# Kernel tuning notes

Hardware: AMD Instinct MI355X
Metric: run time of the kernel (lower is better)

## Reference

```python
import jax, jax.numpy as jnp
import numpy as np

B, C, N = 2, 256, 8192
H = W = 64
C4 = C // 4
EPS = 1e-5


def bn(x, gamma, beta, mean, var):
    # eval-mode batchnorm over channel axis 1
    shape = (1, -1) + (1,) * (x.ndim - 2)
    inv = gamma * jax.lax.rsqrt(var + EPS)
    return x * inv.reshape(shape) + (beta - mean * inv).reshape(shape)


def conv1x1(x, w, b):
    # w: (Cout, Cin)
    return jnp.einsum('bchw,oc->bohw', x, w) + b.reshape(1, -1, 1, 1)


def conv2d(x, w, b=None, padding='VALID', groups=1, lhs_dilation=None):
    y = jax.lax.conv_general_dilated(
        x, w, window_strides=(1, 1), padding=padding,
        lhs_dilation=lhs_dilation, feature_group_count=groups,
        dimension_numbers=('NCHW', 'OIHW', 'NCHW'))
    return y if b is None else y + b.reshape(1, -1, 1, 1)


def lift_net(x, w1, b1, w2, b2, axis):
    # DAWN predictor/updater: ReflectionPad(2,1) -> conv k=4 along axis (C4->2C4)
    # -> ReLU -> 1x1 conv (2C4->C4) -> Tanh
    pad = [(0, 0)] * 4
    pad[axis] = (2, 1)
    xp = jnp.pad(x, pad, mode='reflect')
    k = w1[:, :, None, :] if axis == 3 else w1[:, :, :, None]
    h = jax.nn.relu(conv2d(xp, k, b1))
    return jnp.tanh(conv1x1(h, w2, b2))


def lifting(x, pw, axis):
    # pw = (w1, b1, w2, b2), each with leading net axis [P, U]
    w1, b1, w2, b2 = pw
    sl_e = [slice(None)] * 4; sl_e[axis] = slice(0, None, 2)
    sl_o = [slice(None)] * 4; sl_o[axis] = slice(1, None, 2)
    x_even, x_odd = x[tuple(sl_e)], x[tuple(sl_o)]
    d = x_odd - lift_net(x_even, w1[0], b1[0], w2[0], b2[0], axis)
    c = x_even + lift_net(d, w1[1], b1[1], w2[1], b2[1], axis)
    return c, d


def wavelet2d(x, w1, b1, w2, b2):
    # leading axes of weights: (scheme[horizontal, vertical], net[P, U])
    c, d = lifting(x, (w1[0], b1[0], w2[0], b2[0]), axis=3)  # split along W
    v = (w1[1], b1[1], w2[1], b2[1])                          # shared vertical weights
    LL, LH = lifting(c, v, axis=2)
    HL, HH = lifting(d, v, axis=2)
    return LL, LH, HL, HH


def convT(x, w, b):
    # torch ConvTranspose2d(k=4, stride=2, pad=1); w: (Cin, Cout, 4, 4)
    wc = jnp.flip(w, (2, 3)).transpose(1, 0, 2, 3)  # (Cout, Cin, 4, 4)
    return conv2d(x, wc, b, padding=[(2, 2), (2, 2)], lhs_dilation=(2, 2))


def _forward(tokens, flatten_mat, bn_gamma, bn_beta, bn_mean, bn_var, red_w, red_b,
             lift_w1, lift_b1, lift_w2, lift_b2,
             ff2_w1, ff2_b1, ff2_w2, ff2_b2, ct2_w, ct2_b,
             bn2_gamma, bn2_beta, bn2_mean, bn2_var,
             ff1_w1, ff1_b1, ff1_w2, ff1_b2, ct1_w, ct1_b,
             bn1_gamma, bn1_beta, bn1_mean, bn1_var,
             dw1_w, dw1_b, dw2_w, dw2_b, scale_w, inflate_idx):
    r = bn(tokens, bn_gamma, bn_beta, bn_mean, bn_var)                       # (B,C,N)
    r = jnp.einsum('bmn,bcn->bcm', flatten_mat, r).reshape(B, C, H, W)       # flatten to grid
    rr = conv1x1(r, red_w, red_b)                                            # (B,C/4,H,W)
    LL1, LH1, HL1, HH1 = wavelet2d(rr, lift_w1[0], lift_b1[0], lift_w2[0], lift_b2[0])
    LL2, LH2, HL2, HH2 = wavelet2d(LL1, lift_w1[1], lift_b1[1], lift_w2[1], lift_b2[1])
    x2 = jnp.concatenate([LL2, LH2, HL2, HH2], 1)                            # (B,C,H/4,W/4)
    y2 = conv1x1(jax.nn.gelu(conv1x1(x2, ff2_w1, ff2_b1), approximate=False), ff2_w2, ff2_b2)
    y2 = bn(convT(y2, ct2_w, ct2_b), bn2_gamma, bn2_beta, bn2_mean, bn2_var) # (B,C/2,H/2,W/2)
    x1 = jnp.concatenate([LL1, LH1, HL1, HH1, y2], 1)                        # (B,1.5C,H/2,W/2)
    y1 = conv1x1(jax.nn.gelu(conv1x1(x1, ff1_w1, ff1_b1), approximate=False), ff1_w2, ff1_b2)
    y1 = bn(convT(y1, ct1_w, ct1_b), bn1_gamma, bn1_beta, bn1_mean, bn1_var) # (B,C,H,W)
    r = r + y1
    r = conv2d(r, dw1_w, dw1_b, padding=[(1, 1), (1, 1)], groups=C)          # depthwise 3x3
    r = conv2d(jax.nn.relu(r), dw2_w, dw2_b, padding=[(1, 1), (1, 1)], groups=C)
    r = r.reshape(B, C, H * W) * scale_w.reshape(1, C, 1)                    # grouped 1x1 conv1d
    r = jnp.take_along_axis(r, inflate_idx, axis=2)                          # inflate gather
    return tokens + r


def setup_inputs() -> dict:
    key = jax.random.key(0)
    ks = iter(jax.random.split(key, 64))
    nrm = lambda shape, s=0.05: jax.random.normal(next(ks), shape, jnp.float32) * s
    uni = lambda shape: jax.random.uniform(next(ks), shape, jnp.float32, 0.5, 1.5)
    return dict(
        tokens=jax.random.normal(next(ks), (B, C, N), jnp.float32),
        flatten_mat=nrm((B, H * W, N), 0.02),
        inflate_idx=jax.random.randint(next(ks), (B, C, N), 0, H * W),
        bn_gamma=jnp.ones((C,), jnp.float32), bn_beta=jnp.zeros((C,), jnp.float32),
        bn_mean=nrm((C,), 0.1), bn_var=uni((C,)),
        red_w=nrm((C4, C)), red_b=nrm((C4,)),
        lift_w1=nrm((2, 2, 2, 2 * C4, C4, 4)), lift_b1=nrm((2, 2, 2, 2 * C4)),
        lift_w2=nrm((2, 2, 2, C4, 2 * C4)), lift_b2=nrm((2, 2, 2, C4)),
        ff2_w1=nrm((C, C)), ff2_b1=nrm((C,)), ff2_w2=nrm((C, C)), ff2_b2=nrm((C,)),
        ct2_w=nrm((C, C // 2, 4, 4)), ct2_b=nrm((C // 2,)),
        bn2_gamma=jnp.ones((C // 2,), jnp.float32), bn2_beta=jnp.zeros((C // 2,), jnp.float32),
        bn2_mean=nrm((C // 2,), 0.1), bn2_var=uni((C // 2,)),
        ff1_w1=nrm((C, C + C // 2)), ff1_b1=nrm((C,)), ff1_w2=nrm((C, C)), ff1_b2=nrm((C,)),
        ct1_w=nrm((C, C, 4, 4)), ct1_b=nrm((C,)),
        bn1_gamma=jnp.ones((C,), jnp.float32), bn1_beta=jnp.zeros((C,), jnp.float32),
        bn1_mean=nrm((C,), 0.1), bn1_var=uni((C,)),
        dw1_w=nrm((C, 1, 3, 3)), dw1_b=nrm((C,)),
        dw2_w=nrm((C, 1, 3, 3)), dw2_b=nrm((C,)),
        scale_w=nrm((C,), 0.2),
    )


def reference(tokens, flatten_mat, inflate_idx, bn_gamma, bn_beta, bn_mean, bn_var,
              red_w, red_b, lift_w1, lift_b1, lift_w2, lift_b2,
              ff2_w1, ff2_b1, ff2_w2, ff2_b2, ct2_w, ct2_b,
              bn2_gamma, bn2_beta, bn2_mean, bn2_var,
              ff1_w1, ff1_b1, ff1_w2, ff1_b2, ct1_w, ct1_b,
              bn1_gamma, bn1_beta, bn1_mean, bn1_var,
              dw1_w, dw1_b, dw2_w, dw2_b, scale_w):
    return _forward(tokens, flatten_mat, bn_gamma, bn_beta, bn_mean, bn_var, red_w, red_b,
                    lift_w1, lift_b1, lift_w2, lift_b2,
                    ff2_w1, ff2_b1, ff2_w2, ff2_b2, ct2_w, ct2_b,
                    bn2_gamma, bn2_beta, bn2_mean, bn2_var,
                    ff1_w1, ff1_b1, ff1_w2, ff1_b2, ct1_w, ct1_b,
                    bn1_gamma, bn1_beta, bn1_mean, bn1_var,
                    dw1_w, dw1_b, dw2_w, dw2_b, scale_w, inflate_idx)
```

## Files before the change

kernel.cpp:

```cpp
#include <hip/hip_runtime.h>
#include <math.h>

#define EPSV 1e-5f

typedef __attribute__((ext_vector_type(8))) short bf16x8;
typedef __attribute__((ext_vector_type(4))) float f32x4;
typedef __attribute__((ext_vector_type(8))) unsigned short u16x8;

__device__ inline unsigned short f2bf(float f) {
    unsigned u = __float_as_uint(f);
    unsigned r = (u + 0x7fffu + ((u >> 16) & 1u)) >> 16;
    return (unsigned short)r;
}

__device__ inline float bf2f(unsigned short h) {
    return __uint_as_float(((unsigned)h) << 16);
}

__device__ inline void gload_lds16(const void* g, void* l) {
    __builtin_amdgcn_global_load_lds(
        (const __attribute__((address_space(1))) void*)g,
        (__attribute__((address_space(3))) void*)l, 16, 0, 0);
}

__device__ void wpack_item(const float* __restrict__ w, unsigned short* __restrict__ wp,
                           int Cout, int Cin, int id)
{
    int nc8 = Cin >> 3;
    int cch = id % nc8;
    int rest = id / nc8;
    int o = rest % Cout;
    int pt = rest / Cout;
    if (pt >= 16) return;
    int par = pt >> 2, tap = pt & 3;
    int py = par >> 1, px = par & 1, u = tap >> 1, v = tap & 1;
    int tf = (3 - py - 2 * u) * 4 + (3 - px - 2 * v);
    u16x8 h;
    #pragma unroll
    for (int e = 0; e < 8; ++e)
        h[e] = f2bf(w[((cch * 8 + e) * Cout + o) * 16 + tf]);
    *reinterpret_cast<u16x8*>(&wp[((pt * Cout + o) * Cin) + cch * 8]) = h;
}

__global__ __launch_bounds__(256) void prep_kernel(
    const float4* __restrict__ x, ushort4* __restrict__ y,
    const float* __restrict__ g, const float* __restrict__ be,
    const float* __restrict__ mu, const float* __restrict__ va,
    const float* __restrict__ ct1w, unsigned short* __restrict__ wp1,
    const float* __restrict__ ct2w, unsigned short* __restrict__ wp2)
{
    int vb = blockIdx.x, t = threadIdx.x;
    if (vb < 4096) {
        int i = vb * 256 + t;
        int c = (i >> 11) & 255;
        float s = g[c] * rsqrtf(va[c] + EPSV);
        float tt = be[c] - mu[c] * s;
        float4 v = x[i];
        ushort4 h;
        h.x = f2bf(v.x * s + tt); h.y = f2bf(v.y * s + tt);
        h.z = f2bf(v.z * s + tt); h.w = f2bf(v.w * s + tt);
        y[i] = h;
    } else if (vb < 4608) {
        wpack_item(ct1w, wp1, 256, 256, (vb - 4096) * 256 + t);
    } else {
        wpack_item(ct2w, wp2, 128, 256, (vb - 4608) * 256 + t);
    }
}

__global__ __launch_bounds__(256) void flatten_gemm_mfma(
    const unsigned short* __restrict__ A, const float* __restrict__ Bm,
    float* __restrict__ Pbase)
{
    __shared__ __align__(16) unsigned short AS[4][256 * 32];
    __shared__ __align__(16) unsigned short BS[4][64 * 32];
    const int NTT = 64;
    int t = threadIdx.x;
    int wid = t >> 6, lane = t & 63;
    int fid = blockIdx.z * 64 + blockIdx.x;
    int nid = (fid & 7) * 64 + (fid >> 3);
    int n0 = (nid & 63) * 64;
    int zz = nid >> 6;
    int ks = zz & 3, b = zz >> 2;
    const unsigned short* Ab = A + b * (256 * 8192);
    const float* Bb = Bm + (long)b * (4096 * 8192) + (long)n0 * 8192;
    int k0 = ks * 2048;
    int brow = t >> 3, bc8 = t & 7;
    int l15 = lane & 15, kc = lane >> 4;

    f32x4 acc[4][4] = {};

    auto issueA = [&](int tile) {
        int buf = tile & 3;
        int kb = k0 + tile * 32;
        #pragma unroll
        for (int j = 0; j < 4; ++j) {
            int d16 = (wid * 4 + j) * 64 + lane;
            int row = d16 >> 2;
            int ch = (d16 & 3) ^ ((row >> 1) & 3);
            gload_lds16(Ab + row * 8192 + kb + ch * 8, &AS[buf][(wid * 4 + j) * 512]);
        }
    };
    auto loadB = [&](int tile, float4& f0, float4& f1) {
        int kb = k0 + tile * 32;
        f0 = *(const float4*)(Bb + brow * 8192 + kb + bc8 * 4);
        f1 = *(const float4*)(Bb + (brow + 32) * 8192 + kb + bc8 * 4);
    };
    auto writeB = [&](int tile, const float4& f0, const float4& f1) {
        int buf = tile & 3;
        int ch16 = (bc8 >> 1) ^ ((brow >> 1) & 3);
        ushort4 h;
        h.x = f2bf(f0.x); h.y = f2bf(f0.y); h.z = f2bf(f0.z); h.w = f2bf(f0.w);
        *reinterpret_cast<ushort4*>(&BS[buf][brow * 32 + ch16 * 8 + (bc8 & 1) * 4]) = h;
        int rr2 = brow + 32;
        int ch16b = (bc8 >> 1) ^ ((rr2 >> 1) & 3);
        ushort4 h2;
        h2.x = f2bf(f1.x); h2.y = f2bf(f1.y); h2.z = f2bf(f1.z); h2.w = f2bf(f1.w);
        *reinterpret_cast<ushort4*>(&BS[buf][rr2 * 32 + ch16b * 8 + (bc8 & 1) * 4]) = h2;
    };
    auto mmac = [&](int tile) {
        int buf = tile & 3;
        bf16x8 af[4], bfr[4];
        #pragma unroll
        for (int mf = 0; mf < 4; ++mf) {
            int row = wid * 64 + mf * 16 + l15;
            int ch = kc ^ ((row >> 1) & 3);
            af[mf] = *reinterpret_cast<const bf16x8*>(&AS[buf][row * 32 + ch * 8]);
        }
        #pragma unroll
        for (int nf = 0; nf < 4; ++nf) {
            int row = nf * 16 + l15;
            int ch = kc ^ ((row >> 1) & 3);
            bfr[nf] = *reinterpret_cast<const bf16x8*>(&BS[buf][row * 32 + ch * 8]);
        }
        #pragma unroll
        for (int mf = 0; mf < 4; ++mf)
            #pragma unroll
            for (int nf = 0; nf < 4; ++nf)
                acc[mf][nf] = __builtin_amdgcn_mfma_f32_16x16x32_bf16(
                    af[mf], bfr[nf], acc[mf][nf], 0, 0, 0);
    };

    float4 q00, q01, q10, q11, r0, r1;
    loadB(0, q00, q01);
    loadB(1, q10, q11);
    issueA(0);
    issueA(1);

    for (int tau = 0; tau < NTT; ++tau) {
        writeB(tau, q00, q01);
        if (tau == 0)
            asm volatile("s_waitcnt vmcnt(4) lgkmcnt(0)" ::: "memory");
        else if (tau < NTT - 1)
            asm volatile("s_waitcnt vmcnt(6) lgkmcnt(0)" ::: "memory");
        else
            asm volatile("s_waitcnt vmcnt(0) lgkmcnt(0)" ::: "memory");
        __builtin_amdgcn_s_barrier();
        if (tau + 2 < NTT) {
            loadB(tau + 2, r0, r1);
            issueA(tau + 2);
        }
        mmac(tau);
        q00 = q10; q01 = q11; q10 = r0; q11 = r1;
    }

    float* P = Pbase + (long)ks * 2097152;
    float* Cb = P + (b * 256) * 4096 + n0;
    #pragma unroll
    for (int mf = 0; mf < 4; ++mf) {
        int rbase = wid * 64 + mf * 16 + (lane >> 4) * 4;
        #pragma unroll
        for (int nf = 0; nf < 4; ++nf) {
            int col = nf * 16 + (lane & 15);
            #pragma unroll
            for (int r = 0; r < 4; ++r)
                Cb[(rbase + r) * 4096 + col] = acc[mf][nf][r];
        }
    }
}

__global__ __launch_bounds__(256) void add4_t_kernel(
    const float* __restrict__ p, unsigned short* __restrict__ obf)
{
    __shared__ float tl[64][65];
    int t = threadIdx.x;
    int b = blockIdx.z;
    int c0 = blockIdx.y * 64, p0 = blockIdx.x * 64;
    #pragma unroll
    for (int u = 0; u < 16; ++u) {
        int idx = u * 256 + t;
        int cl = idx >> 6, pl = idx & 63;
        long g = (long)(b * 256 + c0 + cl) * 4096 + p0 + pl;
        tl[cl][pl] = p[g] + p[g + 2097152] + p[g + 2 * 2097152] + p[g + 3 * 2097152];
    }
    __syncthreads();
    #pragma unroll
    for (int u = 0; u < 16; ++u) {
        int idx = u * 256 + t;
        int pl = idx >> 6, cl = idx & 63;
        obf[(long)(b * 4096 + p0 + pl) * 256 + c0 + cl] = f2bf(tl[cl][pl]);
    }
}

template<int NF>
__global__ __launch_bounds__(256) void conv1x1_mfma(
    const unsigned short* __restrict__ xbf, const float* __restrict__ w,
    const float* __restrict__ bias, float* __restrict__ of32,
    unsigned short* __restrict__ obf, int Cin, int Cout, int P, int act)
{
    constexpr int BP = NF * 64;
    __shared__ __align__(16) unsigned short XS[2][BP * 32];
    __shared__ __align__(16) unsigned short WS[2][64 * 32];
    int t = threadIdx.x;
    int wid = t >> 6, lane = t & 63;
    int b = blockIdx.z;
    int p0 = blockIdx.x * BP, o0 = blockIdx.y * 64;
    const unsigned short* xb = xbf + (long)b * P * Cin;
    int wm = t >> 2, wq = t & 3;
    int chunks = Cin >> 5;

    f32x4 acc[4][NF] = {};

    #pragma unroll
    for (int j = 0; j < NF; ++j) {
        int d16 = (wid * NF + j) * 64 + lane;
        int p = d16 >> 2;
        int ch = (d16 & 3) ^ ((p >> 1) & 3);
        gload_lds16(xb + (long)(p0 + p) * Cin + ch * 8, &XS[0][(wid * NF + j) * 512]);
    }
    float4 wr0 = *(const float4*)(w + (o0 + wm) * Cin + wq * 8);
    float4 wr1 = *(const float4*)(w + (o0 + wm) * Cin + wq * 8 + 4);
    __syncthreads();

    for (int cc = 0; cc < chunks; ++cc) {
        int cur = cc & 1;
        {
            int chq = wq ^ ((wm >> 1) & 3);
            u16x8 h;
            h[0] = f2bf(wr0.x); h[1] = f2bf(wr0.y); h[2] = f2bf(wr0.z); h[3] = f2bf(wr0.w);
            h[4] = f2bf(wr1.x); h[5] = f2bf(wr1.y); h[6] = f2bf(wr1.z); h[7] = f2bf(wr1.w);
            *reinterpret_cast<u16x8*>(&WS[cur][wm * 32 + chq * 8]) = h;
        }
        __syncthreads();

        if (cc < chunks - 1) {
            int kn = (cc + 1) * 32;
            #pragma unroll
            for (int j = 0; j < NF; ++j) {
                int d16 = (wid * NF + j) * 64 + lane;
                int p = d16 >> 2;
                int ch = (d16 & 3) ^ ((p >> 1) & 3);
                gload_lds16(xb + (long)(p0 + p) * Cin + kn + ch * 8,
                            &XS[cur ^ 1][(wid * NF + j) * 512]);
            }
            wr0 = *(const float4*)(w + (o0 + wm) * Cin + kn + wq * 8);
            wr1 = *(const float4*)(w + (o0 + wm) * Cin + kn + wq * 8 + 4);
        }

        int l15 = lane & 15, kc = lane >> 4;
        bf16x8 af[4], bfr[NF];
        #pragma unroll
        for (int mf = 0; mf < 4; ++mf) {
            int row = mf * 16 + l15;
            int ch = kc ^ ((row >> 1) & 3);
            af[mf] = *reinterpret_cast<const bf16x8*>(&WS[cur][row * 32 + ch * 8]);
        }
        #pragma unroll
        for (int nf = 0; nf < NF; ++nf) {
            int row = wid * (NF * 16) + nf * 16 + l15;
            int ch = kc ^ ((row >> 1) & 3);
            bfr[nf] = *reinterpret_cast<const bf16x8*>(&XS[cur][row * 32 + ch * 8]);
        }
        #pragma unroll
        for (int mf = 0; mf < 4; ++mf)
            #pragma unroll
            for (int nf = 0; nf < NF; ++nf)
                acc[mf][nf] = __builtin_amdgcn_mfma_f32_16x16x32_bf16(
                    af[mf], bfr[nf], acc[mf][nf], 0, 0, 0);
        __syncthreads();
    }

    int l15 = lane & 15, kc4 = lane >> 4;
    #pragma unroll
    for (int mf = 0; mf < 4; ++mf) {
        #pragma unroll
        for (int nf = 0; nf < NF; ++nf) {
            int p = wid * (NF * 16) + nf * 16 + l15;
            ushort4 hb;
            #pragma unroll
            for (int r = 0; r < 4; ++r) {
                int m = mf * 16 + kc4 * 4 + r;
                float v = acc[mf][nf][r] + bias[o0 + m];
                if (act == 1) v = fmaxf(v, 0.f);
                else if (act == 2) v = 0.5f * v * (1.f + erff(v * 0.70710678118f));
                if (of32) of32[((long)(b * Cout) + o0 + m) * P + p0 + p] = v;
                ((unsigned short*)&hb)[r] = f2bf(v);
            }
            if (obf)
                *reinterpret_cast<ushort4*>(
                    &obf[(long)(b * P + p0 + p) * Cout + o0 + mf * 16 + kc4 * 4]) = hb;
        }
    }
}

__global__ __launch_bounds__(256) void convt_mfma(
    const unsigned short* __restrict__ xbf, const unsigned short* __restrict__ wp,
    const float* __restrict__ bias, const float* __restrict__ g,
    const float* __restrict__ be, const float* __restrict__ mu,
    const float* __restrict__ va, const unsigned short* __restrict__ resbf,
    float* __restrict__ of32, unsigned short* __restrict__ obf,
    int Cin, int Cout, int Hin, int Win, int TR, int cshift, int OCtot, int cof)
{
    __shared__ __align__(16) unsigned short XS[165 * 32];
    __shared__ __align__(16) unsigned short WS[4 * 64 * 32];
    int t = threadIdx.x;
    int wid = t >> 6, lane = t & 63;
    int z = blockIdx.z;
    int b = z >> 2, par = z & 3;
    int py = par >> 1, px = par & 1;
    int o0 = blockIdx.y * 64;
    int i0 = blockIdx.x * TR;
    int CW = Win, CW1 = CW + 1;
    int npatch = (TR + 1) * CW1;
    int Pin = Hin * Win, Pout = 4 * Hin * Win;
    const unsigned short* xb = xbf + (long)b * Pin * Cin;
    int chunks = Cin >> 5;
    int l15 = lane & 15, kc = lane >> 4;

    f32x4 acc[4][2] = {};

    for (int cc = 0; cc < chunks; ++cc) {
        __syncthreads();
        for (int idx = t; idx < npatch * 4; idx += 256) {
            int pp = idx >> 2, ql = idx & 3;
            int qs = ql ^ ((pp >> 1) & 3);
            int a = pp / CW1, bcol = pp - a * CW1;
            int iy = i0 - (1 - py) + a;
            int ix = bcol - (1 - px);
            u16x8 v = {};
            if (iy >= 0 && iy < Hin && ix >= 0 && ix < Win)
                v = *reinterpret_cast<const u16x8*>(
                    &xb[(long)(iy * Win + ix) * Cin + cc * 32 + qs * 8]);
            *reinterpret_cast<u16x8*>(&XS[pp * 32 + ql * 8]) = v;
        }
        {
            int m = t >> 2, q = t & 3;
            int chq = q ^ ((m >> 1) & 3);
            #pragma unroll
            for (int tap = 0; tap < 4; ++tap) {
                u16x8 v = *reinterpret_cast<const u16x8*>(
                    &wp[((long)((par * 4 + tap) * Cout + o0 + m)) * Cin + cc * 32 + q * 8]);
                *reinterpret_cast<u16x8*>(&WS[tap * 2048 + m * 32 + chq * 8]) = v;
            }
        }
        __syncthreads();

        #pragma unroll
        for (int tap = 0; tap < 4; ++tap) {
            int u = tap >> 1, v = tap & 1;
            bf16x8 af[4], bfr[2];
            #pragma unroll
            for (int mf = 0; mf < 4; ++mf) {
                int row = mf * 16 + l15;
                int ch = kc ^ ((row >> 1) & 3);
                af[mf] = *reinterpret_cast<const bf16x8*>(&WS[tap * 2048 + row * 32 + ch * 8]);
            }
            #pragma unroll
            for (int nf = 0; nf < 2; ++nf) {
                int n = wid * 32 + nf * 16 + l15;
                int rn = n >> cshift, cn = n & (CW - 1);
                int pp = (rn + u) * CW1 + cn + v;
                int ch = kc ^ ((pp >> 1) & 3);
                bfr[nf] = *reinterpret_cast<const bf16x8*>(&XS[pp * 32 + ch * 8]);
            }
            #pragma unroll
            for (int mf = 0; mf < 4; ++mf)
                #pragma unroll
                for (int nf = 0; nf < 2; ++nf)
                    acc[mf][nf] = __builtin_amdgcn_mfma_f32_16x16x32_bf16(
                        af[mf], bfr[nf], acc[mf][nf], 0, 0, 0);
        }
    }

    int kc4 = lane >> 4;
    #pragma unroll
    for (int nf = 0; nf < 2; ++nf) {
        int n = wid * 32 + nf * 16 + l15;
        int rn = n >> cshift, cn = n & (CW - 1);
        int y = 2 * (i0 + rn) + py;
        int xx = 2 * cn + px;
        int pout = y * 2 * Win + xx;
        #pragma unroll
        for (int mf = 0; mf < 4; ++mf) {
            ushort4 hb;
            #pragma unroll
            for (int r = 0; r < 4; ++r) {
                int m = mf * 16 + kc4 * 4 + r;
                int o = o0 + m;
                float s = g[o] * rsqrtf(va[o] + EPSV);
                float v = (acc[mf][nf][r] + bias[o]) * s + (be[o] - mu[o] * s);
                if (resbf) v += bf2f(resbf[(long)(b * Pout + pout) * 256 + o]);
                if (of32) of32[((long)(b * Cout) + o) * Pout + pout] = v;
                ((unsigned short*)&hb)[r] = f2bf(v);
            }
            if (obf)
                *reinterpret_cast<ushort4*>(
                    &obf[(long)(b * Pout + pout) * OCtot + cof + o0 + mf * 16 + kc4 * 4]) = hb;
        }
    }
}

__global__ __launch_bounds__(1024) void lift_net_kernel(
    const float* __restrict__ xA, const float* __restrict__ xB,
    const float* __restrict__ oA, const float* __restrict__ oB,
    float* __restrict__ uA, float* __restrict__ uB,
    int x_sB, int x_sC, int x_sR, int x_sA,
    int o_sB, int o_sC, int o_sR, int o_sA,
    int u_sB, int u_sC, int u_sR, int u_sA,
    const float* __restrict__ w1, const float* __restrict__ b1,
    const float* __restrict__ w2, const float* __restrict__ b2,
    int R, int L, int lsh, float sign,
    unsigned short* __restrict__ obf, int Pb, int OCb, int cofA, int cofB)
{
    __shared__ float xsm[4864];
    __shared__ float hsm[8192];
    int t = threadIdx.x;
    int g = t & 63, ocg = t >> 6;
    int b = blockIdx.z;
    int sel = blockIdx.y;
    const float* xin = sel ? xB : xA;
    const float* oth = sel ? oB : oA;
    float* outp = sel ? uB : uA;
    int cofb = sel ? cofB : cofA;
    int rpb = 64 >> lsh;
    int row0 = blockIdx.x * rpb;
    int Lp = L + 3;
    int total = 64 * rpb * Lp;
    for (int idx = t; idx < total; idx += 1024) {
        int c = idx / (rpb * Lp);
        int rem = idx - c * rpb * Lp;
        int rr_l = rem / Lp;
        int q = rem - rr_l * Lp;
        int s = q - 2;
        s = (s < 0) ? -s : s;
        if (s >= L) s = 2 * L - 2 - s;
        xsm[idx] = xin[b * x_sB + c * x_sC + (row0 + rr_l) * x_sR + s * x_sA];
    }
    __syncthreads();

    int ocgu = __builtin_amdgcn_readfirstlane(ocg);
    int rl = g >> lsh, jl = g & (L - 1);
    const float* w1u = w1 + ocgu * 8 * 256;
    float acc1[8] = {};
    for (int c = 0; c < 64; ++c) {
        const float* xr = &xsm[(c * rpb + rl) * Lp + jl];
        float x0 = xr[0], x1 = xr[1], x2 = xr[2], x3 = xr[3];
        const float* wc = w1u + c * 4;
        #pragma unroll
        for (int k = 0; k < 8; ++k) {
            const float* wr = wc + k * 256;
            acc1[k] += wr[0] * x0 + wr[1] * x1 + wr[2] * x2 + wr[3] * x3;
        }
    }
    #pragma unroll
    for (int k = 0; k < 8; ++k) {
        int oc = ocgu * 8 + k;
        hsm[oc * 64 + g] = fmaxf(acc1[k] + b1[oc], 0.f);
    }
    __syncthreads();

    const float* w2u = w2 + ocgu * 4 * 128;
    float acc2[4] = {};
    for (int h4 = 0; h4 < 32; ++h4) {
        float hv0 = hsm[(h4 * 4 + 0) * 64 + g];
        float hv1 = hsm[(h4 * 4 + 1) * 64 + g];
        float hv2 = hsm[(h4 * 4 + 2) * 64 + g];
        float hv3 = hsm[(h4 * 4 + 3) * 64 + g];
        #pragma unroll
        for (int kk = 0; kk < 4; ++kk) {
            const float* wr = w2u + kk * 128 + h4 * 4;
            acc2[kk] += wr[0] * hv0 + wr[1] * hv1 + wr[2] * hv2 + wr[3] * hv3;
        }
    }
    int rg = row0 + rl;
    int p = rg * u_sR + jl * u_sA;
    #pragma unroll
    for (int kk = 0; kk < 4; ++kk) {
        int o = ocgu * 4 + kk;
        float v = oth[b * o_sB + o * o_sC + rg * o_sR + jl * o_sA]
                + sign * tanhf(acc2[kk] + b2[o]);
        outp[b * u_sB + o * u_sC + p] = v;
        if (obf) obf[(long)(b * Pb + p) * OCb + cofb + o] = f2bf(v);
    }
}

__global__ __launch_bounds__(256) void dw_fused_kernel(
    const float* __restrict__ r2, const float* __restrict__ w1, const float* __restrict__ b1,
    const float* __restrict__ w2, const float* __restrict__ b2v,
    const float* __restrict__ scw, const float* __restrict__ tok,
    const int* __restrict__ idx, float* __restrict__ out)
{
    __shared__ float s0[64][68];
    __shared__ float s1[64][68];
    __shared__ float s2[4096];
    int bc = blockIdx.x;
    int c = bc & 255;
    int t = threadIdx.x;
    const float* xp = r2 + (long)bc * 4096;
    for (int i = t; i < 4096; i += 256) s0[i >> 6][i & 63] = xp[i];
    float wa[9], wb[9];
    #pragma unroll
    for (int k = 0; k < 9; ++k) { wa[k] = w1[c * 9 + k]; wb[k] = w2[c * 9 + k]; }
    float ba = b1[c], bb = b2v[c], sc = scw[c];
    __syncthreads();
    for (int i = t; i < 4096; i += 256) {
        int y = i >> 6, x = i & 63;
        float a = ba;
        #pragma unroll
        for (int ky = 0; ky < 3; ++ky) {
            int yy = y + ky - 1;
            if (yy < 0 || yy > 63) continue;
            #pragma unroll
            for (int kx = 0; kx < 3; ++kx) {
                int xx = x + kx - 1;
                if (xx < 0 || xx > 63) continue;
                a += wa[ky * 3 + kx] * s0[yy][xx];
            }
        }
        s1[y][x] = fmaxf(a, 0.f);
    }
    __syncthreads();
    for (int i = t; i < 4096; i += 256) {
        int y = i >> 6, x = i & 63;
        float a = bb;
        #pragma unroll
        for (int ky = 0; ky < 3; ++ky) {
            int yy = y + ky - 1;
            if (yy < 0 || yy > 63) continue;
            #pragma unroll
            for (int kx = 0; kx < 3; ++kx) {
                int xx = x + kx - 1;
                if (xx < 0 || xx > 63) continue;
                a += wb[ky * 3 + kx] * s1[yy][xx];
            }
        }
        s2[i] = a * sc;
    }
    __syncthreads();
    long base = (long)bc << 13;
    const int4* ip = (const int4*)(idx + base);
    const float4* tp = (const float4*)(tok + base);
    float4* op = (float4*)(out + base);
    for (int i = t; i < 2048; i += 256) {
        int4 iv = ip[i];
        float4 tv = tp[i];
        float4 o;
        o.x = tv.x + s2[iv.x];
        o.y = tv.y + s2[iv.y];
        o.z = tv.z + s2[iv.z];
        o.w = tv.w + s2[iv.w];
        op[i] = o;
    }
}

extern "C" void kernel_launch(void* const* d_in, const int* in_sizes, int n_in,
                              void* d_out, int out_size, void* d_ws, size_t ws_size,
                              hipStream_t stream)
{
    const float* tokens = (const float*)d_in[0];
    const float* fm     = (const float*)d_in[1];
    const int*   infl   = (const int*)d_in[2];
    const float* bng = (const float*)d_in[3];
    const float* bnb = (const float*)d_in[4];
    const float* bnm = (const float*)d_in[5];
    const float* bnv = (const float*)d_in[6];
    const float* red_w = (const float*)d_in[7];
    const float* red_b = (const float*)d_in[8];
    const float* lw1 = (const float*)d_in[9];
    const float* lb1 = (const float*)d_in[10];
    const float* lw2 = (const float*)d_in[11];
    const float* lb2 = (const float*)d_in[12];
    const float* f2w1 = (const float*)d_in[13];
    const float* f2b1 = (const float*)d_in[14];
    const float* f2w2 = (const float*)d_in[15];
    const float* f2b2 = (const float*)d_in[16];
    const float* ct2w = (const float*)d_in[17];
    const float* ct2b = (const float*)d_in[18];
    const float* bn2g = (const float*)d_in[19];
    const float* bn2b = (const float*)d_in[20];
    const float* bn2m = (const float*)d_in[21];
    const float* bn2v = (const float*)d_in[22];
    const float* f1w1 = (const float*)d_in[23];
    const float* f1b1 = (const float*)d_in[24];
    const float* f1w2 = (const float*)d_in[25];
    const float* f1b2 = (const float*)d_in[26];
    const float* ct1w = (const float*)d_in[27];
    const float* ct1b = (const float*)d_in[28];
    const float* bn1g = (const float*)d_in[29];
    const float* bn1b = (const float*)d_in[30];
    const float* bn1m = (const float*)d_in[31];
    const float* bn1v = (const float*)d_in[32];
    const float* dw1w = (const float*)d_in[33];
    const float* dw1b = (const float*)d_in[34];
    const float* dw2w = (const float*)d_in[35];
    const float* dw2b = (const float*)d_in[36];
    const float* scw  = (const float*)d_in[37];

    float* ws = (float*)d_ws;
    unsigned short* Abf = (unsigned short*)ws;
    float* part  = ws + 2097152;
    unsigned short* rgrid_bf = (unsigned short*)(ws + 10485760);
    float* rr    = ws + 11534336;
    float* c1    = ws + 12058624;
    float* d1    = ws + 12320768;
    float* c2    = ws + 12582912;
    float* d2    = ws + 12648448;
    float* x2    = ws + 12713984;
    unsigned short* x2_bf  = (unsigned short*)(ws + 12845056);
    float* x1    = ws + 12910592;
    unsigned short* x1_bf  = (unsigned short*)(ws + 13697024);
    unsigned short* g2_bf  = (unsigned short*)(ws + 14090240);
    unsigned short* y2p_bf = (unsigned short*)(ws + 14155776);
    unsigned short* g1_bf  = (unsigned short*)(ws + 14221312);
    unsigned short* y1p_bf = (unsigned short*)(ws + 14483456);
    unsigned short* wp2    = (unsigned short*)(ws + 14745600);
    unsigned short* wp1    = (unsigned short*)(ws + 15007744);
    float* r2 = ws + 15532032;

    prep_kernel<<<4864, 256, 0, stream>>>((const float4*)tokens, (ushort4*)Abf,
                                          bng, bnb, bnm, bnv, ct1w, wp1, ct2w, wp2);
    flatten_gemm_mfma<<<dim3(64, 1, 8), 256, 0, stream>>>(Abf, fm, part);
    add4_t_kernel<<<dim3(64, 4, 2), 256, 0, stream>>>(part, rgrid_bf);
    conv1x1_mfma<2><<<dim3(32, 1, 2), 256, 0, stream>>>(rgrid_bf, red_w, red_b,
                                                        rr, (unsigned short*)nullptr,
                                                        256, 64, 4096, 0);

    auto lift2 = [&](const float* xA, const float* xB, const float* oA, const float* oB,
                     float* uA, float* uB,
                     int xsB, int xsC, int xsR, int xsA,
                     int osB, int osC, int osR, int osA,
                     int usB, int usC, int usR, int usA,
                     int lvl, int sch, int net, int R, int L, float sign,
                     unsigned short* obf, int Pb, int OCb, int cofA, int cofB, int nsel) {
        int widx = (lvl * 2 + sch) * 2 + net;
        int lsh = (L == 32) ? 5 : 4;
        lift_net_kernel<<<dim3(R * L / 64, nsel, 2), 1024, 0, stream>>>(
            xA, xB, oA, oB, uA, uB,
            xsB, xsC, xsR, xsA, osB, osC, osR, osA, usB, usC, usR, usA,
            lw1 + widx * 32768, lb1 + widx * 128, lw2 + widx * 8192, lb2 + widx * 64,
            R, L, lsh, sign, obf, Pb, OCb, cofA, cofB);
    };

    lift2(rr, rr, rr + 1, rr + 1, d1, d1,
          262144, 4096, 64, 2,  262144, 4096, 64, 2,  131072, 2048, 32, 1,
          0, 0, 0, 64, 32, -1.f, nullptr, 0, 0, 0, 0, 1);
    lift2(d1, d1, rr, rr, c1, c1,
          131072, 2048, 32, 1,  262144, 4096, 64, 2,  131072, 2048, 32, 1,
          0, 0, 1, 64, 32, +1.f, nullptr, 0, 0, 0, 0, 1);
    lift2(c1, d1, c1 + 32, d1 + 32, x1 + 65536, x1 + 196608,
          131072, 2048, 1, 64,  131072, 2048, 1, 64,  393216, 1024, 1, 32,
          0, 1, 0, 32, 32, -1.f, x1_bf, 1024, 384, 64, 192, 2);
    lift2(x1 + 65536, x1 + 196608, c1, d1, x1, x1 + 131072,
          393216, 1024, 1, 32,  131072, 2048, 1, 64,  393216, 1024, 1, 32,
          0, 1, 1, 32, 32, +1.f, x1_bf, 1024, 384, 0, 128, 2);
    lift2(x1, x1, x1 + 1, x1 + 1, d2, d2,
          393216, 1024, 32, 2,  393216, 1024, 32, 2,  65536, 512, 16, 1,
          1, 0, 0, 32, 16, -1.f, nullptr, 0, 0, 0, 0, 1);
    lift2(d2, d2, x1, x1, c2, c2,
          65536, 512, 16, 1,  393216, 1024, 32, 2,  65536, 512, 16, 1,
          1, 0, 1, 32, 16, +1.f, nullptr, 0, 0, 0, 0, 1);
    lift2(c2, d2, c2 + 16, d2 + 16, x2 + 16384, x2 + 49152,
          65536, 512, 1, 32,  65536, 512, 1, 32,  65536, 256, 1, 16,
          1, 1, 0, 16, 16, -1.f, x2_bf, 256, 256, 64, 192, 2);
    lift2(x2 + 16384, x2 + 49152, c2, d2, x2, x2 + 32768,
          65536, 256, 1, 16,  65536, 512, 1, 32,  65536, 256, 1, 16,
          1, 1, 1, 16, 16, +1.f, x2_bf, 256, 256, 0, 128, 2);

    conv1x1_mfma<1><<<dim3(4, 4, 2), 256, 0, stream>>>(x2_bf, f2w1, f2b1,
        (float*)nullptr, g2_bf, 256, 256, 256, 2);
    conv1x1_mfma<1><<<dim3(4, 4, 2), 256, 0, stream>>>(g2_bf, f2w2, f2b2,
        (float*)nullptr, y2p_bf, 256, 256, 256, 0);
    convt_mfma<<<dim3(2, 2, 8), 256, 0, stream>>>(y2p_bf, wp2, ct2b,
        bn2g, bn2b, bn2m, bn2v, (const unsigned short*)nullptr,
        (float*)nullptr, x1_bf, 256, 128, 16, 16, 8, 4, 384, 256);

    conv1x1_mfma<2><<<dim3(8, 4, 2), 256, 0, stream>>>(x1_bf, f1w1, f1b1,
        (float*)nullptr, g1_bf, 384, 256, 1024, 2);
    conv1x1_mfma<2><<<dim3(8, 4, 2), 256, 0, stream>>>(g1_bf, f1w2, f1b2,
        (float*)nullptr, y1p_bf, 256, 256, 1024, 0);
    convt_mfma<<<dim3(8, 4, 8), 256, 0, stream>>>(y1p_bf, wp1, ct1b,
        bn1g, bn1b, bn1m, bn1v, rgrid_bf,
        r2, (unsigned short*)nullptr, 256, 256, 32, 32, 4, 5, 0, 0);

    dw_fused_kernel<<<512, 256, 0, stream>>>(r2, dw1w, dw1b, dw2w, dw2b, scw,
                                             tokens, infl, (float*)d_out);
}
```

Measured before the change: 658.9 us.

## Fuse mid-pipeline kernels into one persistent kernel with grid barriers

Replaces the sequence of add4, reduction conv, eight lifting passes, feed-forward convs and both transposed convs with a single 64-block persistent kernel that synchronises stages through an atomic grid barrier. It targets the cost of many small kernel launches and their inter-kernel gaps. In exchange, each stage runs on only 64 workgroups, some of them with idle sub-groups, so parallelism drops for the larger stages such as the final transposed conv. Correctness also depends on all 64 blocks being co-resident.

```diff
diff --git a/kernel.cpp b/kernel.cpp
--- a/kernel.cpp
+++ b/kernel.cpp
@@ -21,6 +21,23 @@
     __builtin_amdgcn_global_load_lds(
         (const __attribute__((address_space(1))) void*)g,
         (__attribute__((address_space(3))) void*)l, 16, 0, 0);
+}
+
+__device__ __forceinline__ void gridbar(unsigned* cnt, unsigned* gen, unsigned nblk)
+{
+    __syncthreads();
+    if (threadIdx.x == 0) {
+        unsigned g = __hip_atomic_load(gen, __ATOMIC_RELAXED, __HIP_MEMORY_SCOPE_AGENT);
+        unsigned a = __hip_atomic_fetch_add(cnt, 1u, __ATOMIC_ACQ_REL, __HIP_MEMORY_SCOPE_AGENT);
+        if (a == nblk - 1u) {
+            __hip_atomic_store(cnt, 0u, __ATOMIC_RELAXED, __HIP_MEMORY_SCOPE_AGENT);
+            __hip_atomic_fetch_add(gen, 1u, __ATOMIC_ACQ_REL, __HIP_MEMORY_SCOPE_AGENT);
+        } else {
+            while (__hip_atomic_load(gen, __ATOMIC_ACQUIRE, __HIP_MEMORY_SCOPE_AGENT) == g)
+                __builtin_amdgcn_s_sleep(8);
+        }
+    }
+    __syncthreads();
 }
 
 __device__ void wpack_item(const float* __restrict__ w, unsigned short* __restrict__ wp,
@@ -47,9 +64,12 @@
     const float* __restrict__ g, const float* __restrict__ be,
     const float* __restrict__ mu, const float* __restrict__ va,
     const float* __restrict__ ct1w, unsigned short* __restrict__ wp1,
-    const float* __restrict__ ct2w, unsigned short* __restrict__ wp2)
+    const float* __restrict__ ct2w, unsigned short* __restrict__ wp2,
+    unsigned* __restrict__ cnt)
 {
     int vb = blockIdx.x, t = threadIdx.x;
+    if (vb == 0 && t == 0)
+        __hip_atomic_store(cnt, 0u, __ATOMIC_RELAXED, __HIP_MEMORY_SCOPE_AGENT);
     if (vb < 4096) {
         int i = vb * 256 + t;
         int c = (i >> 11) & 255;
@@ -178,44 +198,21 @@
     }
 }
 
-__global__ __launch_bounds__(256) void add4_t_kernel(
-    const float* __restrict__ p, unsigned short* __restrict__ obf)
-{
-    __shared__ float tl[64][65];
-    int t = threadIdx.x;
-    int b = blockIdx.z;
-    int c0 = blockIdx.y * 64, p0 = blockIdx.x * 64;
-    #pragma unroll
-    for (int u = 0; u < 16; ++u) {
-        int idx = u * 256 + t;
-        int cl = idx >> 6, pl = idx & 63;
-        long g = (long)(b * 256 + c0 + cl) * 4096 + p0 + pl;
-        tl[cl][pl] = p[g] + p[g + 2097152] + p[g + 2 * 2097152] + p[g + 3 * 2097152];
-    }
-    __syncthreads();
-    #pragma unroll
-    for (int u = 0; u < 16; ++u) {
-        int idx = u * 256 + t;
-        int pl = idx >> 6, cl = idx & 63;
-        obf[(long)(b * 4096 + p0 + pl) * 256 + c0 + cl] = f2bf(tl[cl][pl]);
-    }
-}
-
 template<int NF>
-__global__ __launch_bounds__(256) void conv1x1_mfma(
+__device__ void conv1x1_body(char* sm, int tt,
     const unsigned short* __restrict__ xbf, const float* __restrict__ w,
     const float* __restrict__ bias, float* __restrict__ of32,
-    unsigned short* __restrict__ obf, int Cin, int Cout, int P, int act)
+    unsigned short* __restrict__ obf, int Cin, int Cout, int P, int act,
+    int bx, int by, int bz)
 {
     constexpr int BP = NF * 64;
-    __shared__ __align__(16) unsigned short XS[2][BP * 32];
-    __shared__ __align__(16) unsigned short WS[2][64 * 32];
-    int t = threadIdx.x;
-    int wid = t >> 6, lane = t & 63;
-    int b = blockIdx.z;
-    int p0 = blockIdx.x * BP, o0 = blockIdx.y * 64;
+    unsigned short* XS = (unsigned short*)sm;
+    unsigned short* WS = XS + 2 * BP * 32;
+    int wid = tt >> 6, lane = tt & 63;
+    int b = bz;
+    int p0 = bx * BP, o0 = by * 64;
     const unsigned short* xb = xbf + (long)b * P * Cin;
-    int wm = t >> 2, wq = t & 3;
+    int wm = tt >> 2, wq = tt & 3;
     int chunks = Cin >> 5;
 
     f32x4 acc[4][NF] = {};
@@ -225,7 +222,7 @@
         int d16 = (wid * NF + j) * 64 + lane;
         int p = d16 >> 2;
         int ch = (d16 & 3) ^ ((p >> 1) & 3);
-        gload_lds16(xb + (long)(p0 + p) * Cin + ch * 8, &XS[0][(wid * NF + j) * 512]);
+        gload_lds16(xb + (long)(p0 + p) * Cin + ch * 8, &XS[(wid * NF + j) * 512]);
     }
     float4 wr0 = *(const float4*)(w + (o0 + wm) * Cin + wq * 8);
     float4 wr1 = *(const float4*)(w + (o0 + wm) * Cin + wq * 8 + 4);
@@ -238,7 +235,7 @@
             u16x8 h;
             h[0] = f2bf(wr0.x); h[1] = f2bf(wr0.y); h[2] = f2bf(wr0.z); h[3] = f2bf(wr0.w);
             h[4] = f2bf(wr1.x); h[5] = f2bf(wr1.y); h[6] = f2bf(wr1.z); h[7] = f2bf(wr1.w);
-            *reinterpret_cast<u16x8*>(&WS[cur][wm * 32 + chq * 8]) = h;
+            *reinterpret_cast<u16x8*>(&WS[cur * 2048 + wm * 32 + chq * 8]) = h;
         }
         __syncthreads();
 
@@ -250,7 +247,7 @@
                 int p = d16 >> 2;
                 int ch = (d16 & 3) ^ ((p >> 1) & 3);
                 gload_lds16(xb + (long)(p0 + p) * Cin + kn + ch * 8,
-                            &XS[cur ^ 1][(wid * NF + j) * 512]);
+                            &XS[(cur ^ 1) * BP * 32 + (wid * NF + j) * 512]);
             }
             wr0 = *(const float4*)(w + (o0 + wm) * Cin + kn + wq * 8);
             wr1 = *(const float4*)(w + (o0 + wm) * Cin + kn + wq * 8 + 4);
@@ -262,13 +259,13 @@
         for (int mf = 0; mf < 4; ++mf) {
             int row = mf * 16 + l15;
             int ch = kc ^ ((row >> 1) & 3);
-            af[mf] = *reinterpret_cast<const bf16x8*>(&WS[cur][row * 32 + ch * 8]);
+            af[mf] = *reinterpret_cast<const bf16x8*>(&WS[cur * 2048 + row * 32 + ch * 8]);
         }
         #pragma unroll
         for (int nf = 0; nf < NF; ++nf) {
             int row = wid * (NF * 16) + nf * 16 + l15;
             int ch = kc ^ ((row >> 1) & 3);
-            bfr[nf] = *reinterpret_cast<const bf16x8*>(&XS[cur][row * 32 + ch * 8]);
+            bfr[nf] = *reinterpret_cast<const bf16x8*>(&XS[cur * BP * 32 + row * 32 + ch * 8]);
         }
         #pragma unroll
         for (int mf = 0; mf < 4; ++mf)
@@ -302,23 +299,22 @@
     }
 }
 
-__global__ __launch_bounds__(256) void convt_mfma(
+__device__ void convt_body(char* sm, int tt,
     const unsigned short* __restrict__ xbf, const unsigned short* __restrict__ wp,
     const float* __restrict__ bias, const float* __restrict__ g,
     const float* __restrict__ be, const float* __restrict__ mu,
     const float* __restrict__ va, const unsigned short* __restrict__ resbf,
     float* __restrict__ of32, unsigned short* __restrict__ obf,
-    int Cin, int Cout, int Hin, int Win, int TR, int cshift, int OCtot, int cof)
-{
-    __shared__ __align__(16) unsigned short XS[165 * 32];
-    __shared__ __align__(16) unsigned short WS[4 * 64 * 32];
-    int t = threadIdx.x;
-    int wid = t >> 6, lane = t & 63;
-    int z = blockIdx.z;
-    int b = z >> 2, par = z & 3;
+    int Cin, int Cout, int Hin, int Win, int TR, int cshift, int OCtot, int cof,
+    int bx, int by, int bz)
+{
+    unsigned short* XS = (unsigned short*)sm;
+    unsigned short* WS = XS + 5280;
+    int wid = tt >> 6, lane = tt & 63;
+    int b = bz >> 2, par = bz & 3;
     int py = par >> 1, px = par & 1;
-    int o0 = blockIdx.y * 64;
-    int i0 = blockIdx.x * TR;
+    int o0 = by * 64;
+    int i0 = bx * TR;
     int CW = Win, CW1 = CW + 1;
     int npatch = (TR + 1) * CW1;
     int Pin = Hin * Win, Pout = 4 * Hin * Win;
@@ -330,7 +326,7 @@
 
     for (int cc = 0; cc < chunks; ++cc) {
         __syncthreads();
-        for (int idx = t; idx < npatch * 4; idx += 256) {
+        for (int idx = tt; idx < npatch * 4; idx += 256) {
             int pp = idx >> 2, ql = idx & 3;
             int qs = ql ^ ((pp >> 1) & 3);
             int a = pp / CW1, bcol = pp - a * CW1;
@@ -343,7 +339,7 @@
             *reinterpret_cast<u16x8*>(&XS[pp * 32 + ql * 8]) = v;
         }
         {
-            int m = t >> 2, q = t & 3;
+            int m = tt >> 2, q = tt & 3;
             int chq = q ^ ((m >> 1) & 3);
             #pragma unroll
             for (int tap = 0; tap < 4; ++tap) {
@@ -409,7 +405,7 @@
     }
 }
 
-__global__ __launch_bounds__(1024) void lift_net_kernel(
+__device__ void lift_body(char* sm, int t, int bx, int sel, int bz,
     const float* __restrict__ xA, const float* __restrict__ xB,
     const float* __restrict__ oA, const float* __restrict__ oB,
     float* __restrict__ uA, float* __restrict__ uB,
@@ -418,21 +414,19 @@
     int u_sB, int u_sC, int u_sR, int u_sA,
     const float* __restrict__ w1, const float* __restrict__ b1,
     const float* __restrict__ w2, const float* __restrict__ b2,
-    int R, int L, int lsh, float sign,
+    int L, int lsh, float sign,
     unsigned short* __restrict__ obf, int Pb, int OCb, int cofA, int cofB)
 {
-    __shared__ float xsm[4864];
-    __shared__ float hsm[8192];
-    int t = threadIdx.x;
+    float* xsm = (float*)sm;
+    float* hsm = xsm + 4864;
     int g = t & 63, ocg = t >> 6;
-    int b = blockIdx.z;
-    int sel = blockIdx.y;
+    int b = bz;
     const float* xin = sel ? xB : xA;
     const float* oth = sel ? oB : oA;
     float* outp = sel ? uB : uA;
     int cofb = sel ? cofB : cofA;
     int rpb = 64 >> lsh;
-    int row0 = blockIdx.x * rpb;
+    int row0 = bx * rpb;
     int Lp = L + 3;
     int total = 64 * rpb * Lp;
     for (int idx = t; idx < total; idx += 1024) {
@@ -490,6 +484,156 @@
                 + sign * tanhf(acc2[kk] + b2[o]);
         outp[b * u_sB + o * u_sC + p] = v;
         if (obf) obf[(long)(b * Pb + p) * OCb + cofb + o] = f2bf(v);
+    }
+}
+
+struct MegaArgs {
+    const float* part;
+    unsigned short* rgrid_bf;
+    const float *red_w, *red_b;
+    float *rr, *c1, *d1, *c2, *d2, *x1, *x2;
+    unsigned short *x1_bf, *x2_bf;
+    const float *lw1, *lb1, *lw2, *lb2;
+    const float *f2w1, *f2b1, *f2w2, *f2b2;
+    unsigned short *g2_bf, *y2p_bf;
+    const unsigned short* wp2;
+    const float *ct2b, *bn2g, *bn2b, *bn2m, *bn2v;
+    const float *f1w1, *f1b1, *f1w2, *f1b2;
+    unsigned short *g1_bf, *y1p_bf;
+    const unsigned short* wp1;
+    const float *ct1b, *bn1g, *bn1b, *bn1m, *bn1v;
+    float* r2;
+    unsigned *cnt, *gen;
+};
+
+__global__ __launch_bounds__(1024) void mega_kernel(MegaArgs A)
+{
+    __shared__ __align__(16) char pool[98304];
+    int vb = blockIdx.x;
+    int t = threadIdx.x;
+    int st = t >> 8, tt = t & 255;
+
+    {
+        float* tl = (float*)pool;
+        for (int r = 0; r < 2; ++r) {
+            int task = r * 64 + vb;
+            int b = task >> 6, p0 = (task & 63) * 64;
+            for (int idx = t; idx < 16384; idx += 1024) {
+                int c = idx >> 6, pl = idx & 63;
+                long g = (long)(b * 256 + c) * 4096 + p0 + pl;
+                tl[c * 66 + pl] = A.part[g] + A.part[g + 2097152]
+                                + A.part[g + 2 * 2097152] + A.part[g + 3 * 2097152];
+            }
+            __syncthreads();
+            for (int idx = t; idx < 16384; idx += 1024) {
+                int pl = idx >> 8, c = idx & 255;
+                A.rgrid_bf[(long)(b * 4096 + p0 + pl) * 256 + c] = f2bf(tl[c * 66 + pl]);
+            }
+            __syncthreads();
+        }
+    }
+    gridbar(A.cnt, A.gen, 64);
+
+    if (vb < 16) {
+        int task = vb * 4 + st;
+        conv1x1_body<2>(pool + st * 24576, tt, A.rgrid_bf, A.red_w, A.red_b,
+                        A.rr, nullptr, 256, 64, 4096, 0, task & 31, 0, task >> 5);
+    }
+    gridbar(A.cnt, A.gen, 64);
+
+    #define WSEG(i) A.lw1 + (i) * 32768, A.lb1 + (i) * 128, A.lw2 + (i) * 8192, A.lb2 + (i) * 64
+    lift_body(pool, t, vb & 31, 0, vb >> 5, A.rr, A.rr, A.rr + 1, A.rr + 1, A.d1, A.d1,
+              262144, 4096, 64, 2, 262144, 4096, 64, 2, 131072, 2048, 32, 1,
+              WSEG(0), 32, 5, -1.f, nullptr, 0, 0, 0, 0);
+    gridbar(A.cnt, A.gen, 64);
+    lift_body(pool, t, vb & 31, 0, vb >> 5, A.d1, A.d1, A.rr, A.rr, A.c1, A.c1,
+              131072, 2048, 32, 1, 262144, 4096, 64, 2, 131072, 2048, 32, 1,
+              WSEG(1), 32, 5, +1.f, nullptr, 0, 0, 0, 0);
+    gridbar(A.cnt, A.gen, 64);
+    lift_body(pool, t, vb & 15, (vb >> 4) & 1, vb >> 5,
+              A.c1, A.d1, A.c1 + 32, A.d1 + 32, A.x1 + 65536, A.x1 + 196608,
+              131072, 2048, 1, 64, 131072, 2048, 1, 64, 393216, 1024, 1, 32,
+              WSEG(2), 32, 5, -1.f, A.x1_bf, 1024, 384, 64, 192);
+    gridbar(A.cnt, A.gen, 64);
+    lift_body(pool, t, vb & 15, (vb >> 4) & 1, vb >> 5,
+              A.x1 + 65536, A.x1 + 196608, A.c1, A.d1, A.x1, A.x1 + 131072,
+              393216, 1024, 1, 32, 131072, 2048, 1, 64, 393216, 1024, 1, 32,
+              WSEG(3), 32, 5, +1.f, A.x1_bf, 1024, 384, 0, 128);
+    gridbar(A.cnt, A.gen, 64);
+    if (vb < 16)
+        lift_body(pool, t, vb & 7, 0, vb >> 3, A.x1, A.x1, A.x1 + 1, A.x1 + 1, A.d2, A.d2,
+                  393216, 1024, 32, 2, 393216, 1024, 32, 2, 65536, 512, 16, 1,
+                  WSEG(4), 16, 4, -1.f, nullptr, 0, 0, 0, 0);
+    gridbar(A.cnt, A.gen, 64);
+    if (vb < 16)
+        lift_body(pool, t, vb & 7, 0, vb >> 3, A.d2, A.d2, A.x1, A.x1, A.c2, A.c2,
+                  65536, 512, 16, 1, 393216, 1024, 32, 2, 65536, 512, 16, 1,
+                  WSEG(5), 16, 4, +1.f, nullptr, 0, 0, 0, 0);
+    gridbar(A.cnt, A.gen, 64);
+    if (vb < 16)
+        lift_body(pool, t, vb & 3, (vb >> 2) & 1, vb >> 3,
+                  A.c2, A.d2, A.c2 + 16, A.d2 + 16, A.x2 + 16384, A.x2 + 49152,
+                  65536, 512, 1, 32, 65536, 512, 1, 32, 65536, 256, 1, 16,
+                  WSEG(6), 16, 4, -1.f, A.x2_bf, 256, 256, 64, 192);
+    gridbar(A.cnt, A.gen, 64);
+    if (vb < 16)
+        lift_body(pool, t, vb & 3, (vb >> 2) & 1, vb >> 3,
+                  A.x2 + 16384, A.x2 + 49152, A.c2, A.d2, A.x2, A.x2 + 32768,
+                  65536, 256, 1, 16, 65536, 512, 1, 32, 65536, 256, 1, 16,
+                  WSEG(7), 16, 4, +1.f, A.x2_bf, 256, 256, 0, 128);
+    gridbar(A.cnt, A.gen, 64);
+    #undef WSEG
+
+    if (vb < 8) {
+        int task = vb * 4 + st;
+        conv1x1_body<1>(pool + st * 16384, tt, A.x2_bf, A.f2w1, A.f2b1,
+                        nullptr, A.g2_bf, 256, 256, 256, 2,
+                        task & 3, (task >> 2) & 3, task >> 4);
+    }
+    gridbar(A.cnt, A.gen, 64);
+    if (vb < 8) {
+        int task = vb * 4 + st;
+        conv1x1_body<1>(pool + st * 16384, tt, A.g2_bf, A.f2w2, A.f2b2,
+                        nullptr, A.y2p_bf, 256, 256, 256, 0,
+                        task & 3, (task >> 2) & 3, task >> 4);
+    }
+    gridbar(A.cnt, A.gen, 64);
+    if (vb < 16) {
+        if (st < 2) {
+            int task = vb * 2 + st;
+            convt_body(pool + st * 27008, tt, A.y2p_bf, A.wp2, A.ct2b,
+                       A.bn2g, A.bn2b, A.bn2m, A.bn2v, nullptr,
+                       nullptr, A.x1_bf, 256, 128, 16, 16, 8, 4, 384, 256,
+                       task & 1, (task >> 1) & 1, task >> 2);
+        } else {
+            for (int i = 0; i < 16; ++i) __syncthreads();
+        }
+    }
+    gridbar(A.cnt, A.gen, 64);
+    if (vb < 16) {
+        int task = vb * 4 + st;
+        conv1x1_body<2>(pool + st * 24576, tt, A.x1_bf, A.f1w1, A.f1b1,
+                        nullptr, A.g1_bf, 384, 256, 1024, 2,
+                        task & 7, (task >> 3) & 3, task >> 5);
+    }
+    gridbar(A.cnt, A.gen, 64);
+    if (vb < 16) {
+        int task = vb * 4 + st;
+        conv1x1_body<2>(pool + st * 24576, tt, A.g1_bf, A.f1w2, A.f1b2,
+                        nullptr, A.y1p_bf, 256, 256, 1024, 0,
+                        task & 7, (task >> 3) & 3, task >> 5);
+    }
+    gridbar(A.cnt, A.gen, 64);
+    for (int r = 0; r < 2; ++r) {
+        if (st < 2) {
+            int task = r * 128 + vb * 2 + st;
+            convt_body(pool + st * 27008, tt, A.y1p_bf, A.wp1, A.ct1b,
+                       A.bn1g, A.bn1b, A.bn1m, A.bn1v, A.rgrid_bf,
+                       A.r2, nullptr, 256, 256, 32, 32, 4, 5, 0, 0,
+                       task & 7, (task >> 3) & 3, task >> 5);
+        } else {
+            for (int i = 0; i < 16; ++i) __syncthreads();
+        }
     }
 }
 
@@ -625,72 +769,24 @@
     unsigned short* wp2    = (unsigned short*)(ws + 14745600);
     unsigned short* wp1    = (unsigned short*)(ws + 15007744);
     float* r2 = ws + 15532032;
+    unsigned* bar = (unsigned*)(ws + 17629184);
 
     prep_kernel<<<4864, 256, 0, stream>>>((const float4*)tokens, (ushort4*)Abf,
-                                          bng, bnb, bnm, bnv, ct1w, wp1, ct2w, wp2);
+                                          bng, bnb, bnm, bnv, ct1w, wp1, ct2w, wp2, bar);
     flatten_gemm_mfma<<<dim3(64, 1, 8), 256, 0, stream>>>(Abf, fm, part);
-    add4_t_kernel<<<dim3(64, 4, 2), 256, 0, stream>>>(part, rgrid_bf);
-    conv1x1_mfma<2><<<dim3(32, 1, 2), 256, 0, stream>>>(rgrid_bf, red_w, red_b,
-                                                        rr, (unsigned short*)nullptr,
-                                                        256, 64, 4096, 0);
-
-    auto lift2 = [&](const float* xA, const float* xB, const float* oA, const float* oB,
-                     float* uA, float* uB,
-                     int xsB, int xsC, int xsR, int xsA,
-                     int osB, int osC, int osR, int osA,
-                     int usB, int usC, int usR, int usA,
-                     int lvl, int sch, int net, int R, int L, float sign,
-                     unsigned short* obf, int Pb, int OCb, int cofA, int cofB, int nsel) {
-        int widx = (lvl * 2 + sch) * 2 + net;
-        int lsh = (L == 32) ? 5 : 4;
-        lift_net_kernel<<<dim3(R * L / 64, nsel, 2), 1024, 0, stream>>>(
-            xA, xB, oA, oB, uA, uB,
-            xsB, xsC, xsR, xsA, osB, osC, osR, osA, usB, usC, usR, usA,
-            lw1 + widx * 32768, lb1 + widx * 128, lw2 + widx * 8192, lb2 + widx * 64,
-            R, L, lsh, sign, obf, Pb, OCb, cofA, cofB);
-    };
-
-    lift2(rr, rr, rr + 1, rr + 1, d1, d1,
-          262144, 4096, 64, 2,  262144, 4096, 64, 2,  131072, 2048, 32, 1,
-          0, 0, 0, 64, 32, -1.f, nullptr, 0, 0, 0, 0, 1);
-    lift2(d1, d1, rr, rr, c1, c1,
-          131072, 2048, 32, 1,  262144, 4096, 64, 2,  131072, 2048, 32, 1,
-          0, 0, 1, 64, 32, +1.f, nullptr, 0, 0, 0, 0, 1);
-    lift2(c1, d1, c1 + 32, d1 + 32, x1 + 65536, x1 + 196608,
-          131072, 2048, 1, 64,  131072, 2048, 1, 64,  393216, 1024, 1, 32,
-          0, 1, 0, 32, 32, -1.f, x1_bf, 1024, 384, 64, 192, 2);
-    lift2(x1 + 65536, x1 + 196608, c1, d1, x1, x1 + 131072,
-          393216, 1024, 1, 32,  131072, 2048, 1, 64,  393216, 1024, 1, 32,
-          0, 1, 1, 32, 32, +1.f, x1_bf, 1024, 384, 0, 128, 2);
-    lift2(x1, x1, x1 + 1, x1 + 1, d2, d2,
-          393216, 1024, 32, 2,  393216, 1024, 32, 2,  65536, 512, 16, 1,
-          1, 0, 0, 32, 16, -1.f, nullptr, 0, 0, 0, 0, 1);
-    lift2(d2, d2, x1, x1, c2, c2,
-          65536, 512, 16, 1,  393216, 1024, 32, 2,  65536, 512, 16, 1,
-          1, 0, 1, 32, 16, +1.f, nullptr, 0, 0, 0, 0, 1);
-    lift2(c2, d2, c2 + 16, d2 + 16, x2 + 16384, x2 + 49152,
-          65536, 512, 1, 32,  65536, 512, 1, 32,  65536, 256, 1, 16,
-          1, 1, 0, 16, 16, -1.f, x2_bf, 256, 256, 64, 192, 2);
-    lift2(x2 + 16384, x2 + 49152, c2, d2, x2, x2 + 32768,
-          65536, 256, 1, 16,  65536, 512, 1, 32,  65536, 256, 1, 16,
-          1, 1, 1, 16, 16, +1.f, x2_bf, 256, 256, 0, 128, 2);
-
-    conv1x1_mfma<1><<<dim3(4, 4, 2), 256, 0, stream>>>(x2_bf, f2w1, f2b1,
-        (float*)nullptr, g2_bf, 256, 256, 256, 2);
-    conv1x1_mfma<1><<<dim3(4, 4, 2), 256, 0, stream>>>(g2_bf, f2w2, f2b2,
-        (float*)nullptr, y2p_bf, 256, 256, 256, 0);
-    convt_mfma<<<dim3(2, 2, 8), 256, 0, stream>>>(y2p_bf, wp2, ct2b,
-        bn2g, bn2b, bn2m, bn2v, (const unsigned short*)nullptr,
-        (float*)nullptr, x1_bf, 256, 128, 16, 16, 8, 4, 384, 256);
-
-    conv1x1_mfma<2><<<dim3(8, 4, 2), 256, 0, stream>>>(x1_bf, f1w1, f1b1,
-        (float*)nullptr, g1_bf, 384, 256, 1024, 2);
-    conv1x1_mfma<2><<<dim3(8, 4, 2), 256, 0, stream>>>(g1_bf, f1w2, f1b2,
-        (float*)nullptr, y1p_bf, 256, 256, 1024, 0);
-    convt_mfma<<<dim3(8, 4, 8), 256, 0, stream>>>(y1p_bf, wp1, ct1b,
-        bn1g, bn1b, bn1m, bn1v, rgrid_bf,
-        r2, (unsigned short*)nullptr, 256, 256, 32, 32, 4, 5, 0, 0);
-
+    MegaArgs A;
+    A.part = part; A.rgrid_bf = rgrid_bf; A.red_w = red_w; A.red_b = red_b;
+    A.rr = rr; A.c1 = c1; A.d1 = d1; A.c2 = c2; A.d2 = d2; A.x1 = x1; A.x2 = x2;
+    A.x1_bf = x1_bf; A.x2_bf = x2_bf;
+    A.lw1 = lw1; A.lb1 = lb1; A.lw2 = lw2; A.lb2 = lb2;
+    A.f2w1 = f2w1; A.f2b1 = f2b1; A.f2w2 = f2w2; A.f2b2 = f2b2;
+    A.g2_bf = g2_bf; A.y2p_bf = y2p_bf; A.wp2 = wp2;
+    A.ct2b = ct2b; A.bn2g = bn2g; A.bn2b = bn2b; A.bn2m = bn2m; A.bn2v = bn2v;
+    A.f1w1 = f1w1; A.f1b1 = f1b1; A.f1w2 = f1w2; A.f1b2 = f1b2;
+    A.g1_bf = g1_bf; A.y1p_bf = y1p_bf; A.wp1 = wp1;
+    A.ct1b = ct1b; A.bn1g = bn1g; A.bn1b = bn1b; A.bn1m = bn1m; A.bn1v = bn1v;
+    A.r2 = r2; A.cnt = bar; A.gen = bar + 1;
+    mega_kernel<<<64, 1024, 0, stream>>>(A);
     dw_fused_kernel<<<512, 256, 0, stream>>>(r2, dw1w, dw1b, dw2w, dw2b, scw,
                                              tokens, infl, (float*)d_out);
 }
```

New measurement: 2.166 ms. 229% more time.
